# Performance work log

Measured on AMD Instinct MI355X. Metric: run time of the kernel, lower is better.

The kernel has to match this reference:

```python
import jax, jax.numpy as jnp
import numpy as np

DIM = 768
HEADS = 12
HEAD_DIM = DIM // HEADS
SCALE = HEAD_DIM ** -0.5


def setup_inputs() -> dict:
    key = jax.random.key(0)
    ks = jax.random.split(key, 9)
    B, N, M, C = 4, 1024, 1024, DIM
    std = C ** -0.5
    return {
        "q": jax.random.normal(ks[0], (B, N, C), jnp.float32),
        "k": jax.random.normal(ks[1], (B, M, C), jnp.float32),
        "v": jax.random.normal(ks[2], (B, M, C), jnp.float32),
        "mask": jax.random.uniform(ks[3], (B, N, M), jnp.float32),
        "Wq": jax.random.normal(ks[4], (C, C), jnp.float32) * std,
        "Wk": jax.random.normal(ks[5], (C, C), jnp.float32) * std,
        "Wv": jax.random.normal(ks[6], (C, C), jnp.float32) * std,
        "Wp": jax.random.normal(ks[7], (C, C), jnp.float32) * std,
        "bp": jax.random.normal(ks[8], (C,), jnp.float32) * 0.01,
    }


def reference(q, k, v, mask, Wq, Wk, Wv, Wp, bp):
    B, N, C = q.shape
    M = k.shape[1]
    H, D = HEADS, HEAD_DIM
    qh = (q @ Wq).reshape(B, N, H, D)
    kh = (k @ Wk).reshape(B, M, H, D)
    vh = (v @ Wv).reshape(B, M, H, D)
    attn = jnp.einsum('bnhd,bmhd->bhnm', qh, kh) * SCALE
    attn = jax.nn.softmax(attn, axis=-1)
    # post-softmax multiplicative mask, broadcast over heads
    attn = attn * mask[:, None, :, :]
    x = jnp.einsum('bhnm,bmhd->bnhd', attn, vh).reshape(B, N, C)
    return x @ Wp + bp
```

## Files before the change

### kernel.cpp

```cpp
#include <hip/hip_runtime.h>

typedef __bf16 bf16x8 __attribute__((ext_vector_type(8)));
typedef float f32x4 __attribute__((ext_vector_type(4)));

__device__ __forceinline__ unsigned short f2bf(float f) {
  union { float f; unsigned u; } x; x.f = f;
  unsigned r = x.u + 0x7FFFu + ((x.u >> 16) & 1u);
  return (unsigned short)(r >> 16);
}

__device__ __forceinline__ void gload_lds16(const void* g, void* l) {
  __builtin_amdgcn_global_load_lds(
      (const __attribute__((address_space(1))) unsigned int*)g,
      (__attribute__((address_space(3))) unsigned int*)l, 16, 0, 0);
}

__device__ __forceinline__ f32x4 mfma16(bf16x8 a, bf16x8 b, f32x4 c) {
  return __builtin_amdgcn_mfma_f32_16x16x32_bf16(a, b, c, 0, 0, 0);
}

__device__ __forceinline__ bf16x8 pack8(const f32x4& a, const f32x4& b) {
  bf16x8 r;
  r[0] = (__bf16)a[0]; r[1] = (__bf16)a[1]; r[2] = (__bf16)a[2]; r[3] = (__bf16)a[3];
  r[4] = (__bf16)b[0]; r[5] = (__bf16)b[1]; r[6] = (__bf16)b[2]; r[7] = (__bf16)b[3];
  return r;
}

__global__ __launch_bounds__(256) void conv_qkv(const float* __restrict__ q,
                                                const float* __restrict__ k,
                                                const float* __restrict__ v,
                                                unsigned short* __restrict__ dst) {
  const float* src = (blockIdx.y == 0) ? q : (blockIdx.y == 1 ? k : v);
  size_t i = ((size_t)blockIdx.x * 256 + threadIdx.x) * 4;
  float4 f = *(const float4*)(src + i);
  ushort4 u;
  u.x = f2bf(f.x); u.y = f2bf(f.y); u.z = f2bf(f.z); u.w = f2bf(f.w);
  *(ushort4*)(dst + (size_t)blockIdx.y * (4096u * 768u) + i) = u;
}

__global__ __launch_bounds__(256) void conv_w(const float* __restrict__ W0,
                                              const float* __restrict__ W1,
                                              const float* __restrict__ W2,
                                              const float* __restrict__ W3,
                                              unsigned short* __restrict__ Wt) {
  __shared__ float tile[32][33];
  const float* W = (blockIdx.z == 0) ? W0 : (blockIdx.z == 1) ? W1
                   : (blockIdx.z == 2) ? W2 : W3;
  int tx = threadIdx.x, ty = threadIdx.y;
  int n0 = blockIdx.x * 32, k0 = blockIdx.y * 32;
#pragma unroll
  for (int i = 0; i < 4; ++i)
    tile[ty * 4 + i][tx] = W[(size_t)(k0 + ty * 4 + i) * 768 + n0 + tx];
  __syncthreads();
  unsigned short* o = Wt + (size_t)blockIdx.z * 768 * 768;
#pragma unroll
  for (int i = 0; i < 4; ++i)
    o[(size_t)(n0 + ty * 4 + i) * 768 + k0 + tx] = f2bf(tile[tx][ty * 4 + i]);
}

__device__ __forceinline__ void gemm_core(const unsigned short* __restrict__ A,
                                          const unsigned short* __restrict__ B,
                                          unsigned short (*As)[64 * 64],
                                          unsigned short (*Bs)[128 * 64],
                                          int m0, int n0, int wm, int wn,
                                          int t, int g, int c16,
                                          f32x4 (&acc)[2][4]) {
  auto stageA = [&](unsigned short* dst, int k0) {
#pragma unroll
    for (int i = 0; i < 2; ++i) {
      int fc = i * 256 + t, r = fc >> 3, c = (fc & 7) ^ ((r >> 1) & 7);
      gload_lds16(A + (size_t)(m0 + r) * 768 + k0 + c * 8, (char*)dst + fc * 16);
    }
  };
  auto stageB = [&](unsigned short* dst, int k0) {
#pragma unroll
    for (int i = 0; i < 4; ++i) {
      int fc = i * 256 + t, r = fc >> 3, c = (fc & 7) ^ ((r >> 1) & 7);
      gload_lds16(B + (size_t)(n0 + r) * 768 + k0 + c * 8, (char*)dst + fc * 16);
    }
  };
  stageA(As[0], 0);
  stageB(Bs[0], 0);
  asm volatile("s_waitcnt vmcnt(0)" ::: "memory");
  __syncthreads();
  for (int s = 0; s < 12; ++s) {
    const int cur = s & 1;
    if (s < 11) {
      stageA(As[cur ^ 1], (s + 1) * 64);
      stageB(Bs[cur ^ 1], (s + 1) * 64);
    }
#pragma unroll
    for (int kk = 0; kk < 2; ++kk) {
      const int ch = kk * 4 + g;
      bf16x8 a[2], bw[4];
#pragma unroll
      for (int mi = 0; mi < 2; ++mi) {
        int r = wm + mi * 16 + c16;
        a[mi] = *(const bf16x8*)((char*)As[cur] + r * 128 + (((ch ^ (r >> 1)) & 7) << 4));
      }
#pragma unroll
      for (int ni = 0; ni < 4; ++ni) {
        int r = wn + ni * 16 + c16;
        bw[ni] = *(const bf16x8*)((char*)Bs[cur] + r * 128 + (((ch ^ (r >> 1)) & 7) << 4));
      }
#pragma unroll
      for (int mi = 0; mi < 2; ++mi)
#pragma unroll
        for (int ni = 0; ni < 4; ++ni)
          acc[mi][ni] = mfma16(a[mi], bw[ni], acc[mi][ni]);
    }
    __syncthreads();
  }
}

__global__ __launch_bounds__(256) void gemm_qkv(const unsigned short* __restrict__ Abase,
                                                const unsigned short* __restrict__ Wt,
                                                unsigned short* __restrict__ Hq,
                                                unsigned short* __restrict__ Hk,
                                                unsigned short* __restrict__ Hvt) {
  __shared__ unsigned short As[2][64 * 64], Bs[2][128 * 64];
  const int z = blockIdx.z;
  const unsigned short* A = Abase + (size_t)z * 4096 * 768;
  const unsigned short* B = Wt + (size_t)z * 768 * 768;
  const int t = threadIdx.x, l = t & 63, wid = t >> 6;
  const int g = l >> 4, c16 = l & 15;
  const int m0 = blockIdx.y * 64, n0 = blockIdx.x * 128;
  const int wm = (wid >> 1) * 32, wn = (wid & 1) * 64;
  f32x4 acc[2][4] = {};
  gemm_core(A, B, As, Bs, m0, n0, wm, wn, t, g, c16, acc);
  if (z < 2) {
    const float f = (z == 0) ? 0.125f * 1.44269504088896341f : 1.0f;
    unsigned short* C = (z == 0) ? Hq : Hk;
#pragma unroll
    for (int mi = 0; mi < 2; ++mi)
#pragma unroll
      for (int ni = 0; ni < 4; ++ni) {
        int col = n0 + wn + ni * 16 + c16;
        int row = m0 + wm + mi * 16 + g * 4;
#pragma unroll
        for (int j = 0; j < 4; ++j)
          C[(size_t)(row + j) * 768 + col] = f2bf(acc[mi][ni][j] * f);
      }
  } else {
#pragma unroll
    for (int mi = 0; mi < 2; ++mi) {
      int rowbase = m0 + wm + mi * 16;
      int bat = rowbase >> 10;
      int mloc = (rowbase & 1023) + g * 4;
#pragma unroll
      for (int ni = 0; ni < 4; ++ni) {
        int col = n0 + wn + ni * 16 + c16;
        ushort4 u;
        u.x = f2bf(acc[mi][ni][0]); u.y = f2bf(acc[mi][ni][1]);
        u.z = f2bf(acc[mi][ni][2]); u.w = f2bf(acc[mi][ni][3]);
        *(ushort4*)(Hvt + (((size_t)(bat * 768 + col)) << 10) + mloc) = u;
      }
    }
  }
}

__global__ __launch_bounds__(256) void attn(const unsigned short* __restrict__ qh,
                                            const unsigned short* __restrict__ kh,
                                            const unsigned short* __restrict__ vhT,
                                            const float* __restrict__ mask,
                                            unsigned short* __restrict__ xb) {
  __shared__ unsigned short Ks[3][64 * 64], Vts[3][64 * 64];
  const int flat = blockIdx.x;
  const int lid = (flat & 7) * 96 + (flat >> 3);
  const int h = lid % 12, qt = (lid / 12) & 15, b = lid / 192;
  const int t = threadIdx.x, l = t & 63, wid = t >> 6;
  const int g = l >> 4, c16 = l & 15;

  const unsigned short* qp =
      qh + ((size_t)(b * 1024 + qt * 64 + wid * 16 + c16)) * 768 + h * 64 + g * 8;
  bf16x8 aq0 = *(const bf16x8*)qp;
  bf16x8 aq1 = *(const bf16x8*)(qp + 32);

  const int fc0 = t, r0 = fc0 >> 3, c0 = (fc0 & 7) ^ ((r0 >> 1) & 7);
  const int fc1 = 256 + t, r1 = fc1 >> 3, c1 = (fc1 & 7) ^ ((r1 >> 1) & 7);
  const int s0 = 32 * (r0 >> 5) + 8 * ((r0 >> 2) & 3) + 4 * ((r0 >> 4) & 1) + (r0 & 3);
  const int s1 = 32 * (r1 >> 5) + 8 * ((r1 >> 2) & 3) + 4 * ((r1 >> 4) & 1) + (r1 & 3);
  const unsigned short* kp0 = kh + (size_t)(b * 1024 + s0) * 768 + h * 64 + c0 * 8;
  const unsigned short* kp1 = kh + (size_t)(b * 1024 + s1) * 768 + h * 64 + c1 * 8;
  const unsigned short* vp0 = vhT + ((size_t)(b * 768 + h * 64 + r0)) * 1024 + c0 * 8;
  const unsigned short* vp1 = vhT + ((size_t)(b * 768 + h * 64 + r1)) * 1024 + c1 * 8;

  auto stageKV = [&](int buf) {
    char* kd = (char*)Ks[buf];
    char* vd = (char*)Vts[buf];
    gload_lds16(kp0, kd + fc0 * 16);
    gload_lds16(kp1, kd + fc1 * 16);
    gload_lds16(vp0, vd + fc0 * 16);
    gload_lds16(vp1, vd + fc1 * 16);
    kp0 += 64 * 768; kp1 += 64 * 768; vp0 += 64; vp1 += 64;
  };

  const float* mq = mask + ((size_t)(b * 1024 + qt * 64 + wid * 16 + c16)) * 1024 + 8 * g;

  stageKV(0);
  stageKV(1);
  asm volatile("s_waitcnt vmcnt(4)" ::: "memory");
  __builtin_amdgcn_s_barrier();

  f32x4 o[4] = {};
  f32x4 ls = {0.f, 0.f, 0.f, 0.f};

  for (int kv = 0; kv < 16; ++kv) {
    const int cur = kv % 3;
    if (kv < 14) stageKV((kv + 2) % 3);
    const float* mk = mq + kv * 64;
    f32x4 mreg[4];
    mreg[0] = *(const f32x4*)(mk);
    mreg[1] = *(const f32x4*)(mk + 4);
    mreg[2] = *(const f32x4*)(mk + 32);
    mreg[3] = *(const f32x4*)(mk + 36);
    f32x4 p[4] = {};
#pragma unroll
    for (int kk = 0; kk < 2; ++kk) {
      const int ch = kk * 4 + g;
      bf16x8 aq = kk ? aq1 : aq0;
#pragma unroll
      for (int ni = 0; ni < 4; ++ni) {
        int r = ni * 16 + c16;
        bf16x8 bk = *(const bf16x8*)((char*)Ks[cur] + r * 128 + (((ch ^ (r >> 1)) & 7) << 4));
        p[ni] = mfma16(bk, aq, p[ni]);
      }
    }
#pragma unroll
    for (int ni = 0; ni < 4; ++ni) {
      float e0 = exp2f(p[ni][0]);
      float e1 = exp2f(p[ni][1]);
      float e2 = exp2f(p[ni][2]);
      float e3 = exp2f(p[ni][3]);
      ls[ni] += (e0 + e1) + (e2 + e3);
      p[ni][0] = e0 * mreg[ni][0];
      p[ni][1] = e1 * mreg[ni][1];
      p[ni][2] = e2 * mreg[ni][2];
      p[ni][3] = e3 * mreg[ni][3];
    }
    bf16x8 pa0 = pack8(p[0], p[1]);
    bf16x8 pa1 = pack8(p[2], p[3]);
#pragma unroll
    for (int kk = 0; kk < 2; ++kk) {
      const int ch = kk * 4 + g;
      bf16x8 ap = kk ? pa1 : pa0;
#pragma unroll
      for (int ni = 0; ni < 4; ++ni) {
        int r = ni * 16 + c16;
        bf16x8 bv = *(const bf16x8*)((char*)Vts[cur] + r * 128 + (((ch ^ (r >> 1)) & 7) << 4));
        o[ni] = mfma16(ap, bv, o[ni]);
      }
    }
    if (kv < 14) {
      asm volatile("s_waitcnt vmcnt(4)" ::: "memory");
      __builtin_amdgcn_s_barrier();
    } else if (kv == 14) {
      asm volatile("s_waitcnt vmcnt(0)" ::: "memory");
      __builtin_amdgcn_s_barrier();
    }
  }
  float s = (ls[0] + ls[1]) + (ls[2] + ls[3]);
  s += __shfl_xor(s, 16);
  s += __shfl_xor(s, 32);
  float rinv = 1.0f / s;
  const int rb = (l & 48) | ((l >> 2) & 12);
  float rj[4];
#pragma unroll
  for (int j = 0; j < 4; ++j) rj[j] = __shfl(rinv, rb + j);
#pragma unroll
  for (int ni = 0; ni < 4; ++ni) {
    int col = h * 64 + ni * 16 + c16;
    int row = qt * 64 + wid * 16 + g * 4;
#pragma unroll
    for (int j = 0; j < 4; ++j)
      xb[((size_t)(b * 1024) + row + j) * 768 + col] = f2bf(o[ni][j] * rj[j]);
  }
}

__global__ __launch_bounds__(256) void gemm_proj(const unsigned short* __restrict__ A,
                                                 const unsigned short* __restrict__ B,
                                                 const float* __restrict__ bias,
                                                 float* __restrict__ C) {
  __shared__ unsigned short As[2][64 * 64], Bs[2][128 * 64];
  const int t = threadIdx.x, l = t & 63, wid = t >> 6;
  const int g = l >> 4, c16 = l & 15;
  const int m0 = blockIdx.y * 64, n0 = blockIdx.x * 128;
  const int wm = (wid >> 1) * 32, wn = (wid & 1) * 64;
  f32x4 acc[2][4] = {};
  gemm_core(A, B, As, Bs, m0, n0, wm, wn, t, g, c16, acc);
#pragma unroll
  for (int mi = 0; mi < 2; ++mi)
#pragma unroll
    for (int ni = 0; ni < 4; ++ni) {
      int col = n0 + wn + ni * 16 + c16;
      int row = m0 + wm + mi * 16 + g * 4;
      float bv = bias[col];
#pragma unroll
      for (int j = 0; j < 4; ++j)
        C[(size_t)(row + j) * 768 + col] = acc[mi][ni][j] + bv;
    }
}

extern "C" void kernel_launch(void* const* d_in, const int* in_sizes, int n_in,
                              void* d_out, int out_size, void* d_ws, size_t ws_size,
                              hipStream_t stream) {
  const float* q    = (const float*)d_in[0];
  const float* k    = (const float*)d_in[1];
  const float* v    = (const float*)d_in[2];
  const float* mask = (const float*)d_in[3];
  const float* Wq   = (const float*)d_in[4];
  const float* Wk   = (const float*)d_in[5];
  const float* Wv   = (const float*)d_in[6];
  const float* Wp   = (const float*)d_in[7];
  const float* bp   = (const float*)d_in[8];
  float* out = (float*)d_out;

  const size_t MN = (size_t)4096 * 768;
  const size_t WW = (size_t)768 * 768;
  unsigned short* qkv_bf = (unsigned short*)d_ws;
  unsigned short* wt     = qkv_bf + 3 * MN;
  unsigned short* heads  = wt + 4 * WW;
  unsigned short* xb     = heads + 3 * MN;

  conv_qkv<<<dim3(3072, 3), 256, 0, stream>>>(q, k, v, qkv_bf);
  conv_w<<<dim3(24, 24, 4), dim3(32, 8), 0, stream>>>(Wq, Wk, Wv, Wp, wt);
  gemm_qkv<<<dim3(6, 64, 3), 256, 0, stream>>>(qkv_bf, wt, heads, heads + MN, heads + 2 * MN);
  attn<<<dim3(768, 1, 1), 256, 0, stream>>>(heads, heads + MN, heads + 2 * MN, mask, xb);
  gemm_proj<<<dim3(6, 64), 256, 0, stream>>>(xb, wt + 3 * WW, bp, out);
}
```

Before: 99.47 us.

## Fuse fp32-to-bf16 input conversion into QKV GEMM, prefetch mask, retile projection

Drops the separate conv_qkv kernel. The QKV GEMM now loads fp32 activations into registers, converts them to bf16 and writes them to LDS itself, which saves a full read and write pass over q/k/v. The attention loop prefetches the next mask tile into registers one iteration ahead, double-buffered and unrolled by two. The projection GEMM uses 64x64 tiles, doubling its block count for better occupancy on the CU grid. The costs are more registers for prefetch and fp32 staging, and A loads for the QKV GEMM that no longer bypass VGPRs.

```diff
diff --git a/kernel.cpp b/kernel.cpp
--- a/kernel.cpp
+++ b/kernel.cpp
@@ -24,18 +24,6 @@
   r[0] = (__bf16)a[0]; r[1] = (__bf16)a[1]; r[2] = (__bf16)a[2]; r[3] = (__bf16)a[3];
   r[4] = (__bf16)b[0]; r[5] = (__bf16)b[1]; r[6] = (__bf16)b[2]; r[7] = (__bf16)b[3];
   return r;
-}
-
-__global__ __launch_bounds__(256) void conv_qkv(const float* __restrict__ q,
-                                                const float* __restrict__ k,
-                                                const float* __restrict__ v,
-                                                unsigned short* __restrict__ dst) {
-  const float* src = (blockIdx.y == 0) ? q : (blockIdx.y == 1 ? k : v);
-  size_t i = ((size_t)blockIdx.x * 256 + threadIdx.x) * 4;
-  float4 f = *(const float4*)(src + i);
-  ushort4 u;
-  u.x = f2bf(f.x); u.y = f2bf(f.y); u.z = f2bf(f.z); u.w = f2bf(f.w);
-  *(ushort4*)(dst + (size_t)blockIdx.y * (4096u * 768u) + i) = u;
 }
 
 __global__ __launch_bounds__(256) void conv_w(const float* __restrict__ W0,
@@ -58,76 +46,84 @@
     o[(size_t)(n0 + ty * 4 + i) * 768 + k0 + tx] = f2bf(tile[tx][ty * 4 + i]);
 }
 
-__device__ __forceinline__ void gemm_core(const unsigned short* __restrict__ A,
-                                          const unsigned short* __restrict__ B,
-                                          unsigned short (*As)[64 * 64],
-                                          unsigned short (*Bs)[128 * 64],
-                                          int m0, int n0, int wm, int wn,
-                                          int t, int g, int c16,
-                                          f32x4 (&acc)[2][4]) {
-  auto stageA = [&](unsigned short* dst, int k0) {
-#pragma unroll
-    for (int i = 0; i < 2; ++i) {
-      int fc = i * 256 + t, r = fc >> 3, c = (fc & 7) ^ ((r >> 1) & 7);
-      gload_lds16(A + (size_t)(m0 + r) * 768 + k0 + c * 8, (char*)dst + fc * 16);
-    }
-  };
-  auto stageB = [&](unsigned short* dst, int k0) {
-#pragma unroll
-    for (int i = 0; i < 4; ++i) {
-      int fc = i * 256 + t, r = fc >> 3, c = (fc & 7) ^ ((r >> 1) & 7);
-      gload_lds16(B + (size_t)(n0 + r) * 768 + k0 + c * 8, (char*)dst + fc * 16);
-    }
-  };
-  stageA(As[0], 0);
-  stageB(Bs[0], 0);
-  asm volatile("s_waitcnt vmcnt(0)" ::: "memory");
-  __syncthreads();
-  for (int s = 0; s < 12; ++s) {
-    const int cur = s & 1;
-    if (s < 11) {
-      stageA(As[cur ^ 1], (s + 1) * 64);
-      stageB(Bs[cur ^ 1], (s + 1) * 64);
-    }
-#pragma unroll
-    for (int kk = 0; kk < 2; ++kk) {
-      const int ch = kk * 4 + g;
-      bf16x8 a[2], bw[4];
-#pragma unroll
-      for (int mi = 0; mi < 2; ++mi) {
-        int r = wm + mi * 16 + c16;
-        a[mi] = *(const bf16x8*)((char*)As[cur] + r * 128 + (((ch ^ (r >> 1)) & 7) << 4));
-      }
-#pragma unroll
-      for (int ni = 0; ni < 4; ++ni) {
-        int r = wn + ni * 16 + c16;
-        bw[ni] = *(const bf16x8*)((char*)Bs[cur] + r * 128 + (((ch ^ (r >> 1)) & 7) << 4));
-      }
-#pragma unroll
-      for (int mi = 0; mi < 2; ++mi)
-#pragma unroll
-        for (int ni = 0; ni < 4; ++ni)
-          acc[mi][ni] = mfma16(a[mi], bw[ni], acc[mi][ni]);
-    }
-    __syncthreads();
-  }
-}
-
-__global__ __launch_bounds__(256) void gemm_qkv(const unsigned short* __restrict__ Abase,
+__global__ __launch_bounds__(256) void gemm_qkv(const float* __restrict__ qf,
+                                                const float* __restrict__ kf,
+                                                const float* __restrict__ vf,
                                                 const unsigned short* __restrict__ Wt,
                                                 unsigned short* __restrict__ Hq,
                                                 unsigned short* __restrict__ Hk,
                                                 unsigned short* __restrict__ Hvt) {
   __shared__ unsigned short As[2][64 * 64], Bs[2][128 * 64];
   const int z = blockIdx.z;
-  const unsigned short* A = Abase + (size_t)z * 4096 * 768;
+  const float* A = (z == 0) ? qf : (z == 1) ? kf : vf;
   const unsigned short* B = Wt + (size_t)z * 768 * 768;
   const int t = threadIdx.x, l = t & 63, wid = t >> 6;
   const int g = l >> 4, c16 = l & 15;
   const int m0 = blockIdx.y * 64, n0 = blockIdx.x * 128;
   const int wm = (wid >> 1) * 32, wn = (wid & 1) * 64;
+
+  const int rA0 = t >> 3, cA = t & 7, rA1 = 32 + (t >> 3);
+  float4 fA[4];
+  auto loadA = [&](int k0) {
+    const float* a0 = A + (size_t)(m0 + rA0) * 768 + k0 + cA * 8;
+    const float* a1 = A + (size_t)(m0 + rA1) * 768 + k0 + cA * 8;
+    fA[0] = *(const float4*)a0; fA[1] = *(const float4*)(a0 + 4);
+    fA[2] = *(const float4*)a1; fA[3] = *(const float4*)(a1 + 4);
+  };
+  auto writeA = [&](unsigned short* dst) {
+    bf16x8 b0, b1;
+    b0[0] = (__bf16)fA[0].x; b0[1] = (__bf16)fA[0].y; b0[2] = (__bf16)fA[0].z; b0[3] = (__bf16)fA[0].w;
+    b0[4] = (__bf16)fA[1].x; b0[5] = (__bf16)fA[1].y; b0[6] = (__bf16)fA[1].z; b0[7] = (__bf16)fA[1].w;
+    b1[0] = (__bf16)fA[2].x; b1[1] = (__bf16)fA[2].y; b1[2] = (__bf16)fA[2].z; b1[3] = (__bf16)fA[2].w;
+    b1[4] = (__bf16)fA[3].x; b1[5] = (__bf16)fA[3].y; b1[6] = (__bf16)fA[3].z; b1[7] = (__bf16)fA[3].w;
+    *(bf16x8*)((char*)dst + rA0 * 128 + (((cA ^ (rA0 >> 1)) & 7) << 4)) = b0;
+    *(bf16x8*)((char*)dst + rA1 * 128 + (((cA ^ (rA1 >> 1)) & 7) << 4)) = b1;
+  };
+  auto stageB = [&](unsigned short* dst, int k0) {
+#pragma unroll
+    for (int i = 0; i < 4; ++i) {
+      int fc = i * 256 + t, r = fc >> 3, c = (fc & 7) ^ ((r >> 1) & 7);
+      gload_lds16(B + (size_t)(n0 + r) * 768 + k0 + c * 8, (char*)dst + fc * 16);
+    }
+  };
+
+  loadA(0);
+  stageB(Bs[0], 0);
+  asm volatile("s_waitcnt vmcnt(4)" ::: "memory");
+  writeA(As[0]);
+  __syncthreads();
+
   f32x4 acc[2][4] = {};
-  gemm_core(A, B, As, Bs, m0, n0, wm, wn, t, g, c16, acc);
+  for (int s = 0; s < 12; ++s) {
+    const int cur = s & 1;
+    if (s < 11) { loadA((s + 1) * 64); stageB(Bs[cur ^ 1], (s + 1) * 64); }
+#pragma unroll
+    for (int kk = 0; kk < 2; ++kk) {
+      const int ch = kk * 4 + g;
+      bf16x8 a[2], bw[4];
+#pragma unroll
+      for (int mi = 0; mi < 2; ++mi) {
+        int r = wm + mi * 16 + c16;
+        a[mi] = *(const bf16x8*)((char*)As[cur] + r * 128 + (((ch ^ (r >> 1)) & 7) << 4));
+      }
+#pragma unroll
+      for (int ni = 0; ni < 4; ++ni) {
+        int r = wn + ni * 16 + c16;
+        bw[ni] = *(const bf16x8*)((char*)Bs[cur] + r * 128 + (((ch ^ (r >> 1)) & 7) << 4));
+      }
+#pragma unroll
+      for (int mi = 0; mi < 2; ++mi)
+#pragma unroll
+        for (int ni = 0; ni < 4; ++ni)
+          acc[mi][ni] = mfma16(a[mi], bw[ni], acc[mi][ni]);
+    }
+    if (s < 11) {
+      asm volatile("s_waitcnt vmcnt(4)" ::: "memory");
+      writeA(As[cur ^ 1]);
+    }
+    __syncthreads();
+  }
+
   if (z < 2) {
     const float f = (z == 0) ? 0.125f * 1.44269504088896341f : 1.0f;
     unsigned short* C = (z == 0) ? Hq : Hk;
@@ -197,23 +193,29 @@
 
   const float* mq = mask + ((size_t)(b * 1024 + qt * 64 + wid * 16 + c16)) * 1024 + 8 * g;
 
+  f32x4 o[4] = {};
+  f32x4 ls = {0.f, 0.f, 0.f, 0.f};
+  f32x4 mA[4], mB[4];
+
   stageKV(0);
   stageKV(1);
-  asm volatile("s_waitcnt vmcnt(4)" ::: "memory");
+  mA[0] = *(const f32x4*)(mq);
+  mA[1] = *(const f32x4*)(mq + 4);
+  mA[2] = *(const f32x4*)(mq + 32);
+  mA[3] = *(const f32x4*)(mq + 36);
+  asm volatile("s_waitcnt vmcnt(0)" ::: "memory");
   __builtin_amdgcn_s_barrier();
 
-  f32x4 o[4] = {};
-  f32x4 ls = {0.f, 0.f, 0.f, 0.f};
-
-  for (int kv = 0; kv < 16; ++kv) {
+  auto iter = [&](int kv, f32x4 (&mc)[4], f32x4 (&mn)[4]) {
     const int cur = kv % 3;
+    if (kv < 15) {
+      const float* mk = mq + (kv + 1) * 64;
+      mn[0] = *(const f32x4*)(mk);
+      mn[1] = *(const f32x4*)(mk + 4);
+      mn[2] = *(const f32x4*)(mk + 32);
+      mn[3] = *(const f32x4*)(mk + 36);
+    }
     if (kv < 14) stageKV((kv + 2) % 3);
-    const float* mk = mq + kv * 64;
-    f32x4 mreg[4];
-    mreg[0] = *(const f32x4*)(mk);
-    mreg[1] = *(const f32x4*)(mk + 4);
-    mreg[2] = *(const f32x4*)(mk + 32);
-    mreg[3] = *(const f32x4*)(mk + 36);
     f32x4 p[4] = {};
 #pragma unroll
     for (int kk = 0; kk < 2; ++kk) {
@@ -233,10 +235,10 @@
       float e2 = exp2f(p[ni][2]);
       float e3 = exp2f(p[ni][3]);
       ls[ni] += (e0 + e1) + (e2 + e3);
-      p[ni][0] = e0 * mreg[ni][0];
-      p[ni][1] = e1 * mreg[ni][1];
-      p[ni][2] = e2 * mreg[ni][2];
-      p[ni][3] = e3 * mreg[ni][3];
+      p[ni][0] = e0 * mc[ni][0];
+      p[ni][1] = e1 * mc[ni][1];
+      p[ni][2] = e2 * mc[ni][2];
+      p[ni][3] = e3 * mc[ni][3];
     }
     bf16x8 pa0 = pack8(p[0], p[1]);
     bf16x8 pa1 = pack8(p[2], p[3]);
@@ -258,7 +260,13 @@
       asm volatile("s_waitcnt vmcnt(0)" ::: "memory");
       __builtin_amdgcn_s_barrier();
     }
-  }
+  };
+
+  for (int kv2 = 0; kv2 < 16; kv2 += 2) {
+    iter(kv2, mA, mB);
+    iter(kv2 + 1, mB, mA);
+  }
+
   float s = (ls[0] + ls[1]) + (ls[2] + ls[3]);
   s += __shfl_xor(s, 16);
   s += __shfl_xor(s, 32);
@@ -281,17 +289,57 @@
                                                  const unsigned short* __restrict__ B,
                                                  const float* __restrict__ bias,
                                                  float* __restrict__ C) {
-  __shared__ unsigned short As[2][64 * 64], Bs[2][128 * 64];
+  __shared__ unsigned short As[2][64 * 64], Bs[2][64 * 64];
   const int t = threadIdx.x, l = t & 63, wid = t >> 6;
   const int g = l >> 4, c16 = l & 15;
-  const int m0 = blockIdx.y * 64, n0 = blockIdx.x * 128;
-  const int wm = (wid >> 1) * 32, wn = (wid & 1) * 64;
-  f32x4 acc[2][4] = {};
-  gemm_core(A, B, As, Bs, m0, n0, wm, wn, t, g, c16, acc);
+  const int m0 = blockIdx.y * 64, n0 = blockIdx.x * 64;
+  const int wm = (wid >> 1) * 32, wn = (wid & 1) * 32;
+  auto stage = [&](unsigned short* dst, const unsigned short* src, int k0) {
+#pragma unroll
+    for (int i = 0; i < 2; ++i) {
+      int fc = i * 256 + t, r = fc >> 3, c = (fc & 7) ^ ((r >> 1) & 7);
+      gload_lds16(src + (size_t)r * 768 + k0 + c * 8, (char*)dst + fc * 16);
+    }
+  };
+  const unsigned short* Abase = A + (size_t)m0 * 768;
+  const unsigned short* Bbase = B + (size_t)n0 * 768;
+  stage(As[0], Abase, 0);
+  stage(Bs[0], Bbase, 0);
+  asm volatile("s_waitcnt vmcnt(0)" ::: "memory");
+  __syncthreads();
+  f32x4 acc[2][2] = {};
+  for (int s = 0; s < 12; ++s) {
+    const int cur = s & 1;
+    if (s < 11) {
+      stage(As[cur ^ 1], Abase, (s + 1) * 64);
+      stage(Bs[cur ^ 1], Bbase, (s + 1) * 64);
+    }
+#pragma unroll
+    for (int kk = 0; kk < 2; ++kk) {
+      const int ch = kk * 4 + g;
+      bf16x8 a[2], bw[2];
+#pragma unroll
+      for (int mi = 0; mi < 2; ++mi) {
+        int r = wm + mi * 16 + c16;
+        a[mi] = *(const bf16x8*)((char*)As[cur] + r * 128 + (((ch ^ (r >> 1)) & 7) << 4));
+      }
+#pragma unroll
+      for (int ni = 0; ni < 2; ++ni) {
+        int r = wn + ni * 16 + c16;
+        bw[ni] = *(const bf16x8*)((char*)Bs[cur] + r * 128 + (((ch ^ (r >> 1)) & 7) << 4));
+      }
+#pragma unroll
+      for (int mi = 0; mi < 2; ++mi)
+#pragma unroll
+        for (int ni = 0; ni < 2; ++ni)
+          acc[mi][ni] = mfma16(a[mi], bw[ni], acc[mi][ni]);
+    }
+    __syncthreads();
+  }
 #pragma unroll
   for (int mi = 0; mi < 2; ++mi)
 #pragma unroll
-    for (int ni = 0; ni < 4; ++ni) {
+    for (int ni = 0; ni < 2; ++ni) {
       int col = n0 + wn + ni * 16 + c16;
       int row = m0 + wm + mi * 16 + g * 4;
       float bv = bias[col];
@@ -317,14 +365,12 @@
 
   const size_t MN = (size_t)4096 * 768;
   const size_t WW = (size_t)768 * 768;
-  unsigned short* qkv_bf = (unsigned short*)d_ws;
-  unsigned short* wt     = qkv_bf + 3 * MN;
-  unsigned short* heads  = wt + 4 * WW;
-  unsigned short* xb     = heads + 3 * MN;
-
-  conv_qkv<<<dim3(3072, 3), 256, 0, stream>>>(q, k, v, qkv_bf);
+  unsigned short* wt    = (unsigned short*)d_ws;
+  unsigned short* heads = wt + 4 * WW;
+  unsigned short* xb    = heads + 3 * MN;
+
   conv_w<<<dim3(24, 24, 4), dim3(32, 8), 0, stream>>>(Wq, Wk, Wv, Wp, wt);
-  gemm_qkv<<<dim3(6, 64, 3), 256, 0, stream>>>(qkv_bf, wt, heads, heads + MN, heads + 2 * MN);
+  gemm_qkv<<<dim3(6, 64, 3), 256, 0, stream>>>(q, k, v, wt, heads, heads + MN, heads + 2 * MN);
   attn<<<dim3(768, 1, 1), 256, 0, stream>>>(heads, heads + MN, heads + 2 * MN, mask, xb);
-  gemm_proj<<<dim3(6, 64), 256, 0, stream>>>(xb, wt + 3 * WW, bp, out);
-}
+  gemm_proj<<<dim3(12, 64), 256, 0, stream>>>(xb, wt + 3 * WW, bp, out);
+}
```

Measured after the change: 114.0 us. 14.6% more time.
